# Performance work log

Hardware: AMD Instinct MI355X
Metric: run time of the kernel (lower is better)

The kernel has to match this reference:

```python
import jax, jax.numpy as jnp
import numpy as np

K, OUT, IN = 4, 4096, 4096
B, S = 2, 2048

def setup_inputs() -> dict:
    key = jax.random.key(0)
    k1, k2, k3 = jax.random.split(key, 3)
    x = jax.random.normal(k1, (B, S, IN), dtype=jnp.float32)
    alphas = jax.random.normal(k2, (K,), dtype=jnp.float32)
    # binary bases in {-1, +1}, stored as int8 like the torch buffer
    bases = (jax.random.randint(k3, (K, OUT, IN), 0, 2) * 2 - 1).astype(jnp.int8)
    return {"x": x, "alphas": alphas, "bases": bases}

def reference(x, alphas, bases):
    # W_q = sum_i alphas[i] * bases[i]  -> [out, in]
    W_q = jnp.einsum('k,koi->oi', alphas, bases.astype(x.dtype))
    # y = x @ W_q.T  -> [B, S, out]
    return jnp.einsum('bsi,oi->bso', x, W_q)
```

## Files before the change

### kernel.cpp

```cpp
#include <hip/hip_runtime.h>
#include <hip/hip_bf16.h>
#include <stdint.h>

#define DIM_M 4096
#define DIM_N 4096
#define DIM_K 4096
#define NBASE 4
#define BASE_STRIDE (DIM_N * DIM_K)

typedef __bf16 bf16x8 __attribute__((ext_vector_type(8)));
typedef float floatx4 __attribute__((ext_vector_type(4)));
typedef unsigned short ushort8 __attribute__((ext_vector_type(8)));

typedef const __attribute__((address_space(1))) void* gptr1;
typedef __attribute__((address_space(3))) void* lptr3;

__device__ __forceinline__ void async_copy16(const void* g, void* l) {
    __builtin_amdgcn_global_load_lds((gptr1)g, (lptr3)l, 16, 0, 0);
}

__device__ __forceinline__ unsigned short f2bf(float f) {
    uint32_t u = __float_as_uint(f);
    uint32_t r = (u + 0x7FFFu + ((u >> 16) & 1u)) >> 16;
    return (unsigned short)r;
}

__global__ __launch_bounds__(256) void prep_kernel(
        const int* __restrict__ bases, const float* __restrict__ alphas,
        const float* __restrict__ x,
        unsigned short* __restrict__ Wb, unsigned short* __restrict__ Xb) {
    const int bid = blockIdx.x;
    if (bid < 8192) {
        const long e = ((long)bid * 256 + threadIdx.x) * 8;
        const float a0 = alphas[0], a1 = alphas[1], a2 = alphas[2], a3 = alphas[3];
        const int4 p0 = *(const int4*)(bases + e);
        const int4 p1 = *(const int4*)(bases + e + 4);
        const int4 q0 = *(const int4*)(bases + BASE_STRIDE + e);
        const int4 q1 = *(const int4*)(bases + BASE_STRIDE + e + 4);
        const int4 r0 = *(const int4*)(bases + 2L * BASE_STRIDE + e);
        const int4 r1 = *(const int4*)(bases + 2L * BASE_STRIDE + e + 4);
        const int4 s0 = *(const int4*)(bases + 3L * BASE_STRIDE + e);
        const int4 s1 = *(const int4*)(bases + 3L * BASE_STRIDE + e + 4);
        ushort8 o;
        o[0] = f2bf(a0 * p0.x + a1 * q0.x + a2 * r0.x + a3 * s0.x);
        o[1] = f2bf(a0 * p0.y + a1 * q0.y + a2 * r0.y + a3 * s0.y);
        o[2] = f2bf(a0 * p0.z + a1 * q0.z + a2 * r0.z + a3 * s0.z);
        o[3] = f2bf(a0 * p0.w + a1 * q0.w + a2 * r0.w + a3 * s0.w);
        o[4] = f2bf(a0 * p1.x + a1 * q1.x + a2 * r1.x + a3 * s1.x);
        o[5] = f2bf(a0 * p1.y + a1 * q1.y + a2 * r1.y + a3 * s1.y);
        o[6] = f2bf(a0 * p1.z + a1 * q1.z + a2 * r1.z + a3 * s1.z);
        o[7] = f2bf(a0 * p1.w + a1 * q1.w + a2 * r1.w + a3 * s1.w);
        *(ushort8*)(Wb + e) = o;
    } else {
        const long e = ((long)(bid - 8192) * 256 + threadIdx.x) * 8;
        const float4 v0 = *(const float4*)(x + e);
        const float4 v1 = *(const float4*)(x + e + 4);
        ushort8 o;
        o[0] = f2bf(v0.x); o[1] = f2bf(v0.y); o[2] = f2bf(v0.z); o[3] = f2bf(v0.w);
        o[4] = f2bf(v1.x); o[5] = f2bf(v1.y); o[6] = f2bf(v1.z); o[7] = f2bf(v1.w);
        *(ushort8*)(Xb + e) = o;
    }
}

__global__ __launch_bounds__(256) void gemm_bt_kernel(
        const unsigned short* __restrict__ A, const unsigned short* __restrict__ Bt,
        float* __restrict__ C) {
    __shared__ unsigned short sA[128 * 32];
    __shared__ unsigned short sB[128 * 32];

    const int t = threadIdx.x;
    const int wave = t >> 6, lane = t & 63;
    const int wm = (wave >> 1) * 64;
    const int wn = (wave & 1) * 64;
    const int quad = lane >> 4, l16 = lane & 15;

    const int mBase = blockIdx.y * 128;
    const int nBase = blockIdx.x * 128;

    const int srow = t >> 2;
    const int qc = (t & 3) ^ ((t >> 3) & 3);
    const unsigned short* gA0 = A + (size_t)(mBase + srow) * DIM_K + qc * 8;
    const unsigned short* gA1 = gA0 + (size_t)64 * DIM_K;
    const unsigned short* gB0 = Bt + (size_t)(nBase + srow) * DIM_K + qc * 8;
    const unsigned short* gB1 = gB0 + (size_t)64 * DIM_K;
    unsigned short* lA0 = sA + t * 8;
    unsigned short* lA1 = sA + 2048 + t * 8;
    unsigned short* lB0 = sB + t * 8;
    unsigned short* lB1 = sB + 2048 + t * 8;

    const int swz = quad ^ ((l16 >> 1) & 3);
    const int aoff0 = (wm + l16) * 32 + swz * 8;
    const int boff0 = (wn + l16) * 32 + swz * 8;

    floatx4 acc[4][4] = {};

    for (int kt = 0; kt < DIM_K; kt += 32) {
        async_copy16(gA0, lA0);
        async_copy16(gA1, lA1);
        async_copy16(gB0, lB0);
        async_copy16(gB1, lB1);
        gA0 += 32; gA1 += 32; gB0 += 32; gB1 += 32;
        __syncthreads();

        bf16x8 a[4], b[4];
#pragma unroll
        for (int i = 0; i < 4; i++)
            a[i] = *(const bf16x8*)(sA + aoff0 + i * 16 * 32);
#pragma unroll
        for (int j = 0; j < 4; j++)
            b[j] = *(const bf16x8*)(sB + boff0 + j * 16 * 32);

#pragma unroll
        for (int i = 0; i < 4; i++)
#pragma unroll
            for (int j = 0; j < 4; j++)
                acc[i][j] = __builtin_amdgcn_mfma_f32_16x16x32_bf16(
                    a[i], b[j], acc[i][j], 0, 0, 0);

        __syncthreads();
    }

#pragma unroll
    for (int i = 0; i < 4; i++) {
#pragma unroll
        for (int j = 0; j < 4; j++) {
#pragma unroll
            for (int r = 0; r < 4; r++) {
                const int row = mBase + wm + i * 16 + quad * 4 + r;
                const int col = nBase + wn + j * 16 + l16;
                C[(size_t)row * DIM_N + col] = acc[i][j][r];
            }
        }
    }
}

__global__ __launch_bounds__(256) void naive_kernel(
        const float* __restrict__ x, const float* __restrict__ alphas,
        const int* __restrict__ bases, float* __restrict__ out) {
    const long o = (long)blockIdx.x * 256 + threadIdx.x;
    const int m = (int)(o >> 12), n = (int)(o & 4095);
    const float a0 = alphas[0], a1 = alphas[1], a2 = alphas[2], a3 = alphas[3];
    const float* xr = x + (long)m * DIM_K;
    const int* b0 = bases + (long)n * DIM_K;
    const int* b1 = b0 + BASE_STRIDE;
    const int* b2 = b1 + BASE_STRIDE;
    const int* b3 = b2 + BASE_STRIDE;
    float acc = 0.f;
    for (int i = 0; i < DIM_K; i++) {
        float w = a0 * b0[i] + a1 * b1[i] + a2 * b2[i] + a3 * b3[i];
        acc += xr[i] * w;
    }
    out[o] = acc;
}

extern "C" void kernel_launch(void* const* d_in, const int* in_sizes, int n_in,
                              void* d_out, int out_size, void* d_ws, size_t ws_size,
                              hipStream_t stream) {
    const float* x      = (const float*)d_in[0];
    const float* alphas = (const float*)d_in[1];
    const int*   bases  = (const int*)d_in[2];
    float* out = (float*)d_out;

    const size_t need = (size_t)2 * DIM_N * DIM_K + (size_t)2 * DIM_M * DIM_K;
    if (ws_size >= need) {
        unsigned short* Wb = (unsigned short*)d_ws;
        unsigned short* Xb = (unsigned short*)d_ws + (size_t)DIM_N * DIM_K;
        prep_kernel<<<16384, 256, 0, stream>>>(bases, alphas, x, Wb, Xb);
        gemm_bt_kernel<<<dim3(DIM_N / 128, DIM_M / 128), 256, 0, stream>>>(Xb, Wb, out);
    } else {
        naive_kernel<<<(DIM_M * DIM_N) / 256, 256, 0, stream>>>(x, alphas, bases, out);
    }
}
```

Baseline: 599.2 us.

## Double-buffer GEMM LDS tiles with register-staged prefetch of next K-slice

Replaces direct global-to-LDS async copies with a software pipeline. Each thread loads the next K tile into registers, computes MFMAs on the current LDS buffer, then writes the registers into the alternate LDS buffer, so there is one barrier per iteration instead of two. The aim is to hide global load latency behind the MFMA work. In exchange it uses twice the LDS and extra VGPRs, and adds explicit LDS store instructions.

```diff
diff --git a/kernel.cpp b/kernel.cpp
--- a/kernel.cpp
+++ b/kernel.cpp
@@ -5,19 +5,11 @@
 #define DIM_M 4096
 #define DIM_N 4096
 #define DIM_K 4096
-#define NBASE 4
 #define BASE_STRIDE (DIM_N * DIM_K)
 
 typedef __bf16 bf16x8 __attribute__((ext_vector_type(8)));
 typedef float floatx4 __attribute__((ext_vector_type(4)));
 typedef unsigned short ushort8 __attribute__((ext_vector_type(8)));
-
-typedef const __attribute__((address_space(1))) void* gptr1;
-typedef __attribute__((address_space(3))) void* lptr3;
-
-__device__ __forceinline__ void async_copy16(const void* g, void* l) {
-    __builtin_amdgcn_global_load_lds((gptr1)g, (lptr3)l, 16, 0, 0);
-}
 
 __device__ __forceinline__ unsigned short f2bf(float f) {
     uint32_t u = __float_as_uint(f);
@@ -65,8 +57,8 @@
 __global__ __launch_bounds__(256) void gemm_bt_kernel(
         const unsigned short* __restrict__ A, const unsigned short* __restrict__ Bt,
         float* __restrict__ C) {
-    __shared__ unsigned short sA[128 * 32];
-    __shared__ unsigned short sB[128 * 32];
+    __shared__ unsigned short sA[2 * 128 * 32];
+    __shared__ unsigned short sB[2 * 128 * 32];
 
     const int t = threadIdx.x;
     const int wave = t >> 6, lane = t & 63;
@@ -83,10 +75,6 @@
     const unsigned short* gA1 = gA0 + (size_t)64 * DIM_K;
     const unsigned short* gB0 = Bt + (size_t)(nBase + srow) * DIM_K + qc * 8;
     const unsigned short* gB1 = gB0 + (size_t)64 * DIM_K;
-    unsigned short* lA0 = sA + t * 8;
-    unsigned short* lA1 = sA + 2048 + t * 8;
-    unsigned short* lB0 = sB + t * 8;
-    unsigned short* lB1 = sB + 2048 + t * 8;
 
     const int swz = quad ^ ((l16 >> 1) & 3);
     const int aoff0 = (wm + l16) * 32 + swz * 8;
@@ -94,21 +82,37 @@
 
     floatx4 acc[4][4] = {};
 
+    ushort8 rA0 = *(const ushort8*)gA0;
+    ushort8 rA1 = *(const ushort8*)gA1;
+    ushort8 rB0 = *(const ushort8*)gB0;
+    ushort8 rB1 = *(const ushort8*)gB1;
+    gA0 += 32; gA1 += 32; gB0 += 32; gB1 += 32;
+    *(ushort8*)(sA + t * 8) = rA0;
+    *(ushort8*)(sA + 2048 + t * 8) = rA1;
+    *(ushort8*)(sB + t * 8) = rB0;
+    *(ushort8*)(sB + 2048 + t * 8) = rB1;
+    __syncthreads();
+
+    int p = 0;
     for (int kt = 0; kt < DIM_K; kt += 32) {
-        async_copy16(gA0, lA0);
-        async_copy16(gA1, lA1);
-        async_copy16(gB0, lB0);
-        async_copy16(gB1, lB1);
-        gA0 += 32; gA1 += 32; gB0 += 32; gB1 += 32;
-        __syncthreads();
+        const bool more = (kt + 32) < DIM_K;
+        if (more) {
+            rA0 = *(const ushort8*)gA0;
+            rA1 = *(const ushort8*)gA1;
+            rB0 = *(const ushort8*)gB0;
+            rB1 = *(const ushort8*)gB1;
+            gA0 += 32; gA1 += 32; gB0 += 32; gB1 += 32;
+        }
 
+        const unsigned short* bufA = sA + p * 4096;
+        const unsigned short* bufB = sB + p * 4096;
         bf16x8 a[4], b[4];
 #pragma unroll
         for (int i = 0; i < 4; i++)
-            a[i] = *(const bf16x8*)(sA + aoff0 + i * 16 * 32);
+            a[i] = *(const bf16x8*)(bufA + aoff0 + i * 16 * 32);
 #pragma unroll
         for (int j = 0; j < 4; j++)
-            b[j] = *(const bf16x8*)(sB + boff0 + j * 16 * 32);
+            b[j] = *(const bf16x8*)(bufB + boff0 + j * 16 * 32);
 
 #pragma unroll
         for (int i = 0; i < 4; i++)
@@ -117,7 +121,16 @@
                 acc[i][j] = __builtin_amdgcn_mfma_f32_16x16x32_bf16(
                     a[i], b[j], acc[i][j], 0, 0, 0);
 
+        if (more) {
+            unsigned short* wA = sA + (p ^ 1) * 4096;
+            unsigned short* wB = sB + (p ^ 1) * 4096;
+            *(ushort8*)(wA + t * 8) = rA0;
+            *(ushort8*)(wA + 2048 + t * 8) = rA1;
+            *(ushort8*)(wB + t * 8) = rB0;
+            *(ushort8*)(wB + 2048 + t * 8) = rB1;
+        }
         __syncthreads();
+        p ^= 1;
     }
 
 #pragma unroll
```

New measurement: 599.4 us. No clear change (+0.0%).
